# Performance work log

Hardware: AMD Instinct MI355X
Metric: run time of the kernel (lower is better)

Reference implementation:

```python
import jax, jax.numpy as jnp
import numpy as np

# ---- static config (mirrors init_kwargs) ----
BATCH = 16384
N_SCALARS = 64
N_KERNELS = 32
L2_INDICES = tuple(range(15))
N_L2 = len(L2_INDICES) + 1          # selected kernels + sum-over-kernels
HIDDEN_MIX = 256
HIDDEN_CORR = 128
SILU_NORM = 1.6790                   # e3nn normalize2mom constant for silu

# ---- real-basis Wigner 3j tensors (unit Frobenius norm, as in e3nn) ----
def _su2_gen(l):
    m = np.arange(-l, l + 1)
    d = 2 * l + 1
    Jz = np.diag(m).astype(complex)
    jp = np.sqrt(l * (l + 1) - m[:-1] * (m[:-1] + 1))
    Jp = np.zeros((d, d), complex)
    Jp[np.arange(1, d), np.arange(0, d - 1)] = jp
    Jm = Jp.conj().T
    return (Jp + Jm) / 2, (Jp - Jm) / 2j, Jz

def _real_basis(l):
    d = 2 * l + 1
    U = np.zeros((d, d), complex)
    U[l, l] = 1.0
    for m in range(1, l + 1):
        U[l + m, l + m] = (-1) ** m / np.sqrt(2)
        U[l + m, l - m] = 1 / np.sqrt(2)
        U[l - m, l - m] = 1j / np.sqrt(2)
        U[l - m, l + m] = -1j * (-1) ** m / np.sqrt(2)
    return U

def _real_gens(l):
    if l == 0:
        return [np.zeros((1, 1))] * 3
    U = _real_basis(l)
    return [np.real(U @ (-1j * J) @ U.conj().T) for J in _su2_gen(l)]

def _w3j(l1, l2, l3):
    G1, G2, G3 = _real_gens(l1), _real_gens(l2), _real_gens(l3)
    d1, d2, d3 = 2 * l1 + 1, 2 * l2 + 1, 2 * l3 + 1
    I1, I2, I3 = np.eye(d1), np.eye(d2), np.eye(d3)
    rows = []
    for a in range(3):  # invariance under all 3 so(3) generators
        rows.append(np.kron(np.kron(G1[a], I2), I3)
                    + np.kron(np.kron(I1, G2[a]), I3)
                    + np.kron(np.kron(I1, I2), G3[a]))
    M = np.concatenate(rows, 0)
    _, _, Vh = np.linalg.svd(M)
    c = Vh[-1].reshape(d1, d2, d3)
    c = c / np.linalg.norm(c)
    idx = np.unravel_index(np.argmax(np.abs(c)), c.shape)
    return (c * np.sign(c[idx])).astype(np.float32)

C000 = jnp.asarray(_w3j(0, 0, 0))
C022 = jnp.asarray(_w3j(0, 2, 2))
C202 = jnp.asarray(_w3j(2, 0, 2))
C220 = jnp.asarray(_w3j(2, 2, 0))
C222 = jnp.asarray(_w3j(2, 2, 2))

def _tp_path(w, c, x1, x2):
    # w: [u,v,w], c (wigner 3j): [i,j,k], x1: [b,u,i], x2: [b,v,j] -> [b,w,k]
    return jnp.einsum('uvw,ijk,bui,bvj->bwk', w, c, x1, x2, optimize='optimal')

def _forward(scalars, kernel_t2s, mlp_w1, mlp_w2, mlp_w3, gate_threshold,
             tp1_w000, tp1_w220, tp1_w022, tp1_w202, tp1_w222,
             tp2_w022, tp2_w202, tp2_w222, correction_scale):
    # ---- KernelMixingHead ----
    h = SILU_NORM * jax.nn.silu(scalars @ mlp_w1 / mlp_w1.shape[0] ** 0.5)
    h = SILU_NORM * jax.nn.silu(h @ mlp_w2 / mlp_w2.shape[0] ** 0.5)
    relative = h @ mlp_w3 / mlp_w3.shape[0] ** 0.5          # [B, K]
    magnitude = jnp.linalg.norm(kernel_t2s, axis=-1)         # [B, K]
    gate = magnitude / (magnitude + gate_threshold)
    weights = relative * gate / N_KERNELS ** 0.5
    mixed = jnp.einsum('bk,bkm->bm', weights, kernel_t2s)    # [B, 5]

    # ---- EquivariantCorrectionHead ----
    sel = kernel_t2s[:, jnp.asarray(L2_INDICES), :]          # [B, n_l2-1, 5]
    t = jnp.concatenate([sel, kernel_t2s.sum(axis=1, keepdims=True)], axis=1)  # [B, N_L2, 5]
    xs = scalars[:, :, None]                                 # [B, ns, 1] (0e channels)
    ns, nl, hc = N_SCALARS, N_L2, HIDDEN_CORR
    # e3nn FullyConnectedTensorProduct path norms ('component'/'element')
    a0 = (1.0 / (ns * ns + nl * nl)) ** 0.5
    a2 = (5.0 / (2 * ns * nl + nl * nl)) ** 0.5
    y0 = a0 * (_tp_path(tp1_w000, C000, xs, xs) + _tp_path(tp1_w220, C220, t, t))   # [B,hc,1]
    y2 = a2 * (_tp_path(tp1_w022, C022, xs, t) + _tp_path(tp1_w202, C202, t, xs)
               + _tp_path(tp1_w222, C222, t, t))                                     # [B,hc,5]
    b2 = (5.0 / (3 * hc * hc)) ** 0.5
    corr = b2 * (_tp_path(tp2_w022, C022, y0, y2) + _tp_path(tp2_w202, C202, y2, y0)
                 + _tp_path(tp2_w222, C222, y2, y2))                                 # [B,1,5]
    return mixed + correction_scale * corr[:, 0, :]

def setup_inputs() -> dict:
    key = jax.random.key(0)
    ks = jax.random.split(key, 13)
    f32 = jnp.float32
    return {
        'scalars': jax.random.normal(ks[0], (BATCH, N_SCALARS), f32),
        'kernel_t2s': jax.random.normal(ks[1], (BATCH, N_KERNELS, 5), f32),
        'mlp_w1': jax.random.normal(ks[2], (N_SCALARS, HIDDEN_MIX), f32),
        'mlp_w2': jax.random.normal(ks[3], (HIDDEN_MIX, HIDDEN_MIX), f32),
        'mlp_w3': jax.random.normal(ks[4], (HIDDEN_MIX, N_KERNELS), f32),
        'gate_threshold': jnp.ones((N_KERNELS,), f32),
        'tp1_w000': jax.random.normal(ks[5], (N_SCALARS, N_SCALARS, HIDDEN_CORR), f32),
        'tp1_w220': jax.random.normal(ks[6], (N_L2, N_L2, HIDDEN_CORR), f32),
        'tp1_w022': jax.random.normal(ks[7], (N_SCALARS, N_L2, HIDDEN_CORR), f32),
        'tp1_w202': jax.random.normal(ks[8], (N_L2, N_SCALARS, HIDDEN_CORR), f32),
        'tp1_w222': jax.random.normal(ks[9], (N_L2, N_L2, HIDDEN_CORR), f32),
        'tp2_w022': jax.random.normal(ks[10], (HIDDEN_CORR, HIDDEN_CORR, 1), f32),
        'tp2_w202': jax.random.normal(ks[11], (HIDDEN_CORR, HIDDEN_CORR, 1), f32),
        'tp2_w222': jax.random.normal(ks[12], (HIDDEN_CORR, HIDDEN_CORR, 1), f32),
        'correction_scale': jnp.asarray(0.1, f32),
    }

def reference(scalars, kernel_t2s, mlp_w1, mlp_w2, mlp_w3, gate_threshold,
              tp1_w000, tp1_w220, tp1_w022, tp1_w202, tp1_w222,
              tp2_w022, tp2_w202, tp2_w222, correction_scale):
    return _forward(scalars, kernel_t2s, mlp_w1, mlp_w2, mlp_w3, gate_threshold,
                    tp1_w000, tp1_w220, tp1_w022, tp1_w202, tp1_w222,
                    tp2_w022, tp2_w202, tp2_w222, correction_scale)
```

## Files before the change

### kernel.cpp

```cpp
#include <hip/hip_runtime.h>
#include <hip/hip_bf16.h>
#include <cmath>
#include <complex>
#include <vector>
#include <cstring>
#include <cstdint>


#define C222_FLIP -1.0f

#define MIX_WS_OFF   0
#define W202T_OFF    327680
#define B2H_OFF      393216
#define B2L_OFF      1294336
#define Y0_WS_OFF    2195456
#define Y2P_OFF      10584064

#define NCHUNK2      110

typedef __attribute__((ext_vector_type(8))) short short8;
typedef __attribute__((ext_vector_type(4))) float f32x4;

struct Coefs {
  float c222[125];
  float d022[5];
  float d202[5];
  float d220[5];
  float a0, a2, b2;
};

#define FMA8(acc, wa, wb, sv) do { \
  acc[0] = fmaf((wa).x, (sv), acc[0]); \
  acc[1] = fmaf((wa).y, (sv), acc[1]); \
  acc[2] = fmaf((wa).z, (sv), acc[2]); \
  acc[3] = fmaf((wa).w, (sv), acc[3]); \
  acc[4] = fmaf((wb).x, (sv), acc[4]); \
  acc[5] = fmaf((wb).y, (sv), acc[5]); \
  acc[6] = fmaf((wb).z, (sv), acc[6]); \
  acc[7] = fmaf((wb).w, (sv), acc[7]); \
} while (0)

#define FMA4(acc, wa, sv) do { \
  acc[0] = fmaf((wa).x, (sv), acc[0]); \
  acc[1] = fmaf((wa).y, (sv), acc[1]); \
  acc[2] = fmaf((wa).z, (sv), acc[2]); \
  acc[3] = fmaf((wa).w, (sv), acc[3]); \
} while (0)

__device__ __forceinline__ float act_silu(float x) {
  return 1.679f * x / (1.0f + expf(-x));
}

__device__ __forceinline__ short f2bf(float x) {
  __hip_bfloat16 h = __float2bfloat16(x);
  return *reinterpret_cast<short*>(&h);
}
__device__ __forceinline__ float bf2f(short s) {
  __hip_bfloat16 h = *reinterpret_cast<__hip_bfloat16*>(&s);
  return __bfloat162float(h);
}

__device__ __forceinline__ int bperm(int n, int k) {
  return ((n >> 4) << 9) | (((((k >> 3) << 4) | (n & 15))) << 3) | (k & 7);
}

__global__ __launch_bounds__(256) void k_prep(
    const float* __restrict__ s, const float* __restrict__ t2s,
    const float* __restrict__ w1, const float* __restrict__ w2,
    const float* __restrict__ w3, const float* __restrict__ gthr,
    float* __restrict__ mixed_ws)
{
  __shared__ float sT[64][36];
  __shared__ float hT[256][36];

  const int tid = threadIdx.x;
  const int b0  = blockIdx.x * 32;

  #pragma unroll
  for (int i = 0; i < 8; i++) {
    int flat = tid + i * 256;
    int bl = flat >> 6, k = flat & 63;
    sT[k][bl] = s[(size_t)(b0 + bl) * 64 + k];
  }
  __syncthreads();

  const int cg = tid & 31, bg = tid >> 5;
  const int c0 = cg * 8, bb0 = bg * 4;

  float acc[4][8];
  #pragma unroll
  for (int j = 0; j < 4; j++)
    #pragma unroll
    for (int i = 0; i < 8; i++) acc[j][i] = 0.f;

  for (int k = 0; k < 64; k++) {
    float4 bv = *(const float4*)&sT[k][bb0];
    float4 wa = *(const float4*)&w1[k * 256 + c0];
    float4 wb = *(const float4*)&w1[k * 256 + c0 + 4];
    const float bvv[4] = {bv.x, bv.y, bv.z, bv.w};
    #pragma unroll
    for (int j = 0; j < 4; j++) { FMA8(acc[j], wa, wb, bvv[j]); }
  }
  #pragma unroll
  for (int j = 0; j < 4; j++)
    #pragma unroll
    for (int i = 0; i < 8; i++)
      hT[c0 + i][bb0 + j] = act_silu(acc[j][i] * 0.125f);
  __syncthreads();

  float acc2[4][8];
  #pragma unroll
  for (int j = 0; j < 4; j++)
    #pragma unroll
    for (int i = 0; i < 8; i++) acc2[j][i] = 0.f;

  for (int k = 0; k < 256; k++) {
    float4 bv = *(const float4*)&hT[k][bb0];
    float4 wa = *(const float4*)&w2[k * 256 + c0];
    float4 wb = *(const float4*)&w2[k * 256 + c0 + 4];
    const float bvv[4] = {bv.x, bv.y, bv.z, bv.w};
    #pragma unroll
    for (int j = 0; j < 4; j++) { FMA8(acc2[j], wa, wb, bvv[j]); }
  }
  __syncthreads();
  #pragma unroll
  for (int j = 0; j < 4; j++)
    #pragma unroll
    for (int i = 0; i < 8; i++)
      hT[c0 + i][bb0 + j] = act_silu(acc2[j][i] * 0.0625f);
  __syncthreads();

  const int jj  = tid & 31;
  const int blg = tid >> 5;
  float acc3[4] = {0.f, 0.f, 0.f, 0.f};
  for (int k = 0; k < 256; k++) {
    float wv  = w3[k * 32 + jj];
    float4 hv = *(const float4*)&hT[k][blg * 4];
    acc3[0] = fmaf(hv.x, wv, acc3[0]);
    acc3[1] = fmaf(hv.y, wv, acc3[1]);
    acc3[2] = fmaf(hv.z, wv, acc3[2]);
    acc3[3] = fmaf(hv.w, wv, acc3[3]);
  }
  const float thrv = gthr[jj];
  #pragma unroll
  for (int r = 0; r < 4; r++) {
    int bl = blg * 4 + r;
    int b  = b0 + bl;
    float rel = acc3[r] * 0.0625f;
    const float* tp = t2s + (size_t)(b * 32 + jj) * 5;
    float tv0 = tp[0], tv1 = tp[1], tv2 = tp[2], tv3 = tp[3], tv4 = tp[4];
    float mag  = sqrtf(tv0*tv0 + tv1*tv1 + tv2*tv2 + tv3*tv3 + tv4*tv4);
    float gate = mag / (mag + thrv);
    float w = rel * gate * 0.17677669529663687f;
    float pm0 = w*tv0, pm1 = w*tv1, pm2 = w*tv2, pm3 = w*tv3, pm4 = w*tv4;
    #pragma unroll
    for (int off = 16; off >= 1; off >>= 1) {
      pm0 += __shfl_xor(pm0, off);
      pm1 += __shfl_xor(pm1, off);
      pm2 += __shfl_xor(pm2, off);
      pm3 += __shfl_xor(pm3, off);
      pm4 += __shfl_xor(pm4, off);
    }
    if (jj == 0) {
      float* mp = mixed_ws + (size_t)b * 5;
      mp[0] = pm0; mp[1] = pm1; mp[2] = pm2; mp[3] = pm3; mp[4] = pm4;
    }
  }
}

__global__ __launch_bounds__(256) void k_wprep(
    const float* __restrict__ w000,
    const float* __restrict__ w2022x,
    const float* __restrict__ w2202, float* __restrict__ wSum,
    const float* __restrict__ w022, const float* __restrict__ w202,
    const float* __restrict__ w222, const float* __restrict__ w220,
    short* __restrict__ B2h, short* __restrict__ B2l)
{
  const int tid = threadIdx.x;
  const int blk = blockIdx.x;
  if (blk < 64) {
    int u = blk;
    int base = u * 64 - (u * (u - 1)) / 2;
    int n = (64 - u) * 128;
    for (int idx = tid; idx < n; idx += 256) {
      int t = idx >> 7, wc = idx & 127;
      int v = u + t;
      int p = base + t;
      float val = w000[(size_t)(u * 64 + v) * 128 + wc];
      if (v > u) val += w000[(size_t)(v * 64 + u) * 128 + wc];
      size_t off = (size_t)(45 + (p >> 5)) * 4096 + bperm(wc, p & 31);
      short hs = f2bf(val);
      B2h[off] = hs;
      B2l[off] = f2bf(val - bf2f(hs));
    }
  } else if (blk < 128) {
    int idx = (blk - 64) * 256 + tid;
    int u = idx >> 7, v = idx & 127;
    wSum[v * 128 + u] = w2022x[(size_t)v * 128 + u] + w2202[(size_t)u * 128 + v];
  } else {
    int c = blk - 128;
    #pragma unroll
    for (int i = 0; i < 16; i++) {
      int e = i * 256 + tid;
      int nb = e >> 9;
      int ln = (e >> 3) & 63;
      int j  = e & 7;
      int w  = nb * 16 + (ln & 15);
      int kk = ((ln >> 4) << 3) | j;
      float V = 0.f;
      if (c < 32) {
        int v = c >> 1, u = (c & 1) * 32 + kk;
        V = w022[(size_t)(u * 16 + v) * 128 + w]
          + w202[(size_t)(v * 64 + u) * 128 + w];
      } else if (c < 40) {
        int K = (c - 32) * 32 + kk;
        int u = K >> 4, v = K & 15;
        V = w222[(size_t)(u * 16 + v) * 128 + w];
      } else {
        int q = (c - 40) * 32 + kk;
        if (q < 136) {
          int u = 0;
          while ((u + 1) * 16 - ((u + 1) * u) / 2 <= q) u++;
          int base = u * 16 - (u * (u - 1)) / 2;
          int v = u + (q - base);
          V = w220[(size_t)(u * 16 + v) * 128 + w];
          if (v > u) V += w220[(size_t)(v * 16 + u) * 128 + w];
        }
      }
      short hs = f2bf(V);
      B2h[(size_t)c * 4096 + e] = hs;
      B2l[(size_t)c * 4096 + e] = f2bf(V - bf2f(hs));
    }
  }
}

__global__ __launch_bounds__(512) void k_y2a(
    const float* __restrict__ s, const float* __restrict__ t2s,
    const short* __restrict__ B2h, const short* __restrict__ B2l,
    unsigned short* __restrict__ y2p, Coefs cf)
{
  __shared__ float sL[64][68];
  __shared__ float tL[64][81];
  __shared__ __align__(16) short BhL[2][4096];
  __shared__ __align__(16) short BlL[2][4096];
  __shared__ float cL222[125];

  const int tid  = threadIdx.x;
  const int b0   = blockIdx.x * 64;
  const int wave = tid >> 6;
  const int lane = tid & 63;
  const int m16  = lane & 15;
  const int quad = lane >> 4;
  const int bg   = wave & 3;
  const int nh   = wave >> 2;
  const int bloc = bg * 16 + m16;
  const int wbase = nh * 64;

  float dk022[5];
  #pragma unroll
  for (int k = 0; k < 5; k++) dk022[k] = cf.d022[k];

  if (tid == 0) {
    #pragma unroll
    for (int i = 0; i < 125; i++) cL222[i] = cf.c222[i];
  }
  for (int idx = tid; idx < 4096; idx += 512) {
    int bl = idx >> 6, k = idx & 63;
    sL[bl][k] = s[(size_t)(b0 + bl) * 64 + k];
  }
  for (int idx = tid; idx < 5120; idx += 512) {
    int bl = idx / 80, rem = idx - bl * 80;
    int u = rem / 5, m = rem - u * 5;
    int b = b0 + bl;
    float v;
    if (u < 15) v = t2s[(size_t)(b * 32 + u) * 5 + m];
    else {
      v = 0.f;
      for (int kk = 0; kk < 32; kk++) v += t2s[(size_t)(b * 32 + kk) * 5 + m];
    }
    tL[bl][rem] = v;
  }
  __syncthreads();

  ((short8*)BhL[0])[tid] = ((const short8*)B2h)[tid];
  ((short8*)BlL[0])[tid] = ((const short8*)B2l)[tid];
  __syncthreads();

  f32x4 acc[5][4];
  #pragma unroll
  for (int k = 0; k < 5; k++)
    #pragma unroll
    for (int nf = 0; nf < 4; nf++) acc[k][nf] = 0.f;
  f32x4 p[4];
  #pragma unroll
  for (int nf = 0; nf < 4; nf++) p[nf] = 0.f;

  for (int c = 0; c < 40; c++) {
    const int cur = c & 1;
    if (c + 1 < 40) {
      ((short8*)BhL[cur ^ 1])[tid] = ((const short8*)(B2h + (size_t)(c + 1) * 4096))[tid];
      ((short8*)BlL[cur ^ 1])[tid] = ((const short8*)(B2l + (size_t)(c + 1) * 4096))[tid];
    }
    short8 bhv[4], blv[4];
    #pragma unroll
    for (int nf = 0; nf < 4; nf++) {
      const int nb = nh * 4 + nf;
      bhv[nf] = *(const short8*)&BhL[cur][nb * 512 + lane * 8];
      blv[nf] = *(const short8*)&BlL[cur][nb * 512 + lane * 8];
    }

    if (c < 32) {
      const int ks = c & 1;
      float sv[8];
      {
        float4 a = *(const float4*)&sL[bloc][ks * 32 + quad * 8];
        float4 b = *(const float4*)&sL[bloc][ks * 32 + quad * 8 + 4];
        sv[0]=a.x; sv[1]=a.y; sv[2]=a.z; sv[3]=a.w;
        sv[4]=b.x; sv[5]=b.y; sv[6]=b.z; sv[7]=b.w;
      }
      short8 ah, al;
      #pragma unroll
      for (int j = 0; j < 8; j++) {
        float x = sv[j];
        short hs = f2bf(x);
        ah[j] = hs;
        al[j] = f2bf(x - bf2f(hs));
      }
      #pragma unroll
      for (int nf = 0; nf < 4; nf++) {
        p[nf] = __builtin_amdgcn_mfma_f32_16x16x32_bf16(ah, bhv[nf], p[nf], 0, 0, 0);
        p[nf] = __builtin_amdgcn_mfma_f32_16x16x32_bf16(ah, blv[nf], p[nf], 0, 0, 0);
        p[nf] = __builtin_amdgcn_mfma_f32_16x16x32_bf16(al, bhv[nf], p[nf], 0, 0, 0);
      }
      if (ks == 1) {
        const int v = c >> 1;
        #pragma unroll
        for (int r = 0; r < 4; r++) {
          const int bl = bg * 16 + quad * 4 + r;
          const float* tr = &tL[bl][v * 5];
          #pragma unroll
          for (int k = 0; k < 5; k++) {
            float f = dk022[k] * tr[k];
            #pragma unroll
            for (int nf = 0; nf < 4; nf++)
              acc[k][nf][r] += f * p[nf][r];
          }
        }
        #pragma unroll
        for (int nf = 0; nf < 4; nf++) p[nf] = 0.f;
      }
    } else {
      int cc = c - 32;
      int u  = cc * 2 + (quad >> 1);
      int vb = (quad & 1) * 8;
      float tu[5];
      #pragma unroll
      for (int i = 0; i < 5; i++) tu[i] = tL[bloc][u * 5 + i];
      float G[25];
      #pragma unroll
      for (int jk = 0; jk < 25; jk++) {
        float g = 0.f;
        #pragma unroll
        for (int i = 0; i < 5; i++)
          g = fmaf(cL222[i * 25 + jk], tu[i], g);
        G[jk] = g;
      }
      float av[5][8];
      #pragma unroll
      for (int j = 0; j < 8; j++) {
        float t5[5];
        #pragma unroll
        for (int j5 = 0; j5 < 5; j5++) t5[j5] = tL[bloc][(vb + j) * 5 + j5];
        #pragma unroll
        for (int k = 0; k < 5; k++) {
          float q = 0.f;
          #pragma unroll
          for (int j5 = 0; j5 < 5; j5++)
            q = fmaf(G[j5 * 5 + k], t5[j5], q);
          av[k][j] = q;
        }
      }
      #pragma unroll
      for (int k = 0; k < 5; k++) {
        short8 ah, al;
        #pragma unroll
        for (int j = 0; j < 8; j++) {
          float x = av[k][j];
          short hs = f2bf(x);
          ah[j] = hs;
          al[j] = f2bf(x - bf2f(hs));
        }
        #pragma unroll
        for (int nf = 0; nf < 4; nf++) {
          acc[k][nf] = __builtin_amdgcn_mfma_f32_16x16x32_bf16(ah, bhv[nf], acc[k][nf], 0, 0, 0);
          acc[k][nf] = __builtin_amdgcn_mfma_f32_16x16x32_bf16(ah, blv[nf], acc[k][nf], 0, 0, 0);
          acc[k][nf] = __builtin_amdgcn_mfma_f32_16x16x32_bf16(al, bhv[nf], acc[k][nf], 0, 0, 0);
        }
      }
    }
    __syncthreads();
  }

  #pragma unroll
  for (int nf = 0; nf < 4; nf++) {
    int ch = wbase + nf * 16 + m16;
    #pragma unroll
    for (int r = 0; r < 4; r++) {
      int b = b0 + bg * 16 + quad * 4 + r;
      #pragma unroll
      for (int k = 0; k < 5; k++)
        y2p[((size_t)b * 5 + k) * 128 + ch] = (unsigned short)f2bf(acc[k][nf][r]);
    }
  }
}

__global__ __launch_bounds__(512) void k_y0b(
    const float* __restrict__ s, const float* __restrict__ t2s,
    const short* __restrict__ B2h, const short* __restrict__ B2l,
    float* __restrict__ y0w, Coefs cf)
{
  __shared__ float sL[32][65];
  __shared__ float tL[32][81];
  __shared__ unsigned char p136s[136];
  __shared__ unsigned short p16[2080];

  const int tid  = threadIdx.x;
  const int b0   = blockIdx.x * 32;
  const int wave = tid >> 6;
  const int lane = tid & 63;
  const int m16  = lane & 15;
  const int quad = lane >> 4;
  const int bg   = wave & 1;
  const int nh   = wave >> 1;
  const int bloc = bg * 16 + m16;
  const int wbase = nh * 32;

  float dk220[5];
  #pragma unroll
  for (int k = 0; k < 5; k++) dk220[k] = cf.d220[k];

  for (int idx = tid; idx < 2048; idx += 512) {
    int bl = idx >> 6, k = idx & 63;
    sL[bl][k] = s[(size_t)(b0 + bl) * 64 + k];
  }
  for (int idx = tid; idx < 2560; idx += 512) {
    int bl = idx / 80, rem = idx - bl * 80;
    int u = rem / 5, m = rem - u * 5;
    int b = b0 + bl;
    float v;
    if (u < 15) v = t2s[(size_t)(b * 32 + u) * 5 + m];
    else {
      v = 0.f;
      for (int kk = 0; kk < 32; kk++) v += t2s[(size_t)(b * 32 + kk) * 5 + m];
    }
    tL[bl][rem] = v;
  }
  if (tid < 16) {
    int u = tid;
    int base = u * 16 - (u * (u - 1)) / 2;
    for (int t = 0; t < 16 - u; t++)
      p136s[base + t] = (unsigned char)((u << 4) | (u + t));
  }
  if (tid < 64) {
    int u = tid;
    int base = u * 64 - (u * (u - 1)) / 2;
    for (int t = 0; t < 64 - u; t++)
      p16[base + t] = (unsigned short)((u << 8) | (u + t));
  }
  __syncthreads();

  f32x4 accY0[2];
  accY0[0] = 0.f; accY0[1] = 0.f;

  const short8* Bh8 = (const short8*)B2h;
  const short8* Bl8 = (const short8*)B2l;
  const int off0 = (nh * 2) * 64 + lane;
  const int off1 = off0 + 64;

  for (int c = 40; c < NCHUNK2; c++) {
    const size_t cb = (size_t)c * 512;
    short8 bh0 = Bh8[cb + off0];
    short8 bh1 = Bh8[cb + off1];
    short8 bl0 = Bl8[cb + off0];
    short8 bl1 = Bl8[cb + off1];

    short8 ah, al;
    if (c < 45) {
      int cc = c - 40;
      int qbase = cc * 32 + quad * 8;
      #pragma unroll
      for (int j = 0; j < 8; j++) {
        int q = qbase + j;
        float g = 0.f;
        if (q < 136) {
          int uv = p136s[q];
          int u = uv >> 4, v = uv & 15;
          #pragma unroll
          for (int m = 0; m < 5; m++)
            g = fmaf(dk220[m] * tL[bloc][u * 5 + m], tL[bloc][v * 5 + m], g);
        }
        short hs = f2bf(g);
        ah[j] = hs;
        al[j] = f2bf(g - bf2f(hs));
      }
    } else {
      int pbase = (c - 45) * 32 + quad * 8;
      #pragma unroll
      for (int j = 0; j < 8; j++) {
        int uv = p16[pbase + j];
        float x = sL[bloc][uv >> 8] * sL[bloc][uv & 255];
        short hs = f2bf(x);
        ah[j] = hs;
        al[j] = f2bf(x - bf2f(hs));
      }
    }
    accY0[0] = __builtin_amdgcn_mfma_f32_16x16x32_bf16(ah, bh0, accY0[0], 0, 0, 0);
    accY0[0] = __builtin_amdgcn_mfma_f32_16x16x32_bf16(ah, bl0, accY0[0], 0, 0, 0);
    accY0[0] = __builtin_amdgcn_mfma_f32_16x16x32_bf16(al, bh0, accY0[0], 0, 0, 0);
    accY0[1] = __builtin_amdgcn_mfma_f32_16x16x32_bf16(ah, bh1, accY0[1], 0, 0, 0);
    accY0[1] = __builtin_amdgcn_mfma_f32_16x16x32_bf16(ah, bl1, accY0[1], 0, 0, 0);
    accY0[1] = __builtin_amdgcn_mfma_f32_16x16x32_bf16(al, bh1, accY0[1], 0, 0, 0);
  }

  #pragma unroll
  for (int nf = 0; nf < 2; nf++) {
    int ch = wbase + nf * 16 + m16;
    #pragma unroll
    for (int r = 0; r < 4; r++) {
      int b = b0 + bg * 16 + quad * 4 + r;
      y0w[(size_t)b * 128 + ch] = accY0[nf][r];
    }
  }
}

__global__ __launch_bounds__(512) void k_fused(
    const float* __restrict__ mixed_ws,
    const float* __restrict__ y0w, const unsigned short* __restrict__ y2p,
    const float* __restrict__ wSum, const float* __restrict__ w2222,
    const float* __restrict__ csc, float* __restrict__ out, Coefs cf)
{
  __shared__ __align__(16) float y0I[16][128][2];
  __shared__ __align__(16) float wLd[32][128];
  __shared__ float y2S[5][16][32][2];
  __shared__ float cL222[125];
  __shared__ float corrAcc[32][5];
  __shared__ float pPL[32][25];

  const int tid = threadIdx.x;
  const int b0  = blockIdx.x * 32;

  float dk022[5];
  #pragma unroll
  for (int k = 0; k < 5; k++) dk022[k] = cf.d022[k];

  if (tid == 0) {
    #pragma unroll
    for (int i = 0; i < 125; i++) cL222[i] = cf.c222[i];
  }
  for (int idx = tid; idx < 4096; idx += 512) {
    int bl = idx >> 7, ch = idx & 127;
    y0I[bl >> 1][ch][bl & 1] = cf.a0 * y0w[(size_t)(b0 + bl) * 128 + ch];
  }

  const int xw = tid & 31;
  const int g  = tid >> 5;
  const int w0 = xw * 4;
  const int bA = 2 * g, bB = 2 * g + 1;
  const int srow = tid >> 4;
  const int scol = (tid & 15) * 8;

  float y2acc[5][2][4];
  #pragma unroll
  for (int k = 0; k < 5; k++) {
    #pragma unroll
    for (int h = 0; h < 2; h++) {
      int b = b0 + 2 * g + h;
      const unsigned short* yp = y2p + ((size_t)b * 5 + k) * 128 + w0;
      ushort4 u4 = *(const ushort4*)yp;
      y2acc[k][h][0] = cf.a2 * bf2f((short)u4.x);
      y2acc[k][h][1] = cf.a2 * bf2f((short)u4.y);
      y2acc[k][h][2] = cf.a2 * bf2f((short)u4.z);
      y2acc[k][h][3] = cf.a2 * bf2f((short)u4.w);
    }
  }
  __syncthreads();

  {
    float gvr[2][4] = {{0.f,0.f,0.f,0.f},{0.f,0.f,0.f,0.f}};
    for (int t = 0; t < 4; t++) {
      const int u0 = t * 32;
      *(float4*)&wLd[srow][scol]     = *(const float4*)(wSum + (size_t)(u0 + srow) * 128 + scol);
      *(float4*)&wLd[srow][scol + 4] = *(const float4*)(wSum + (size_t)(u0 + srow) * 128 + scol + 4);
      __syncthreads();
      #pragma unroll 8
      for (int uu = 0; uu < 32; uu++) {
        float2 y0p = *(const float2*)&y0I[g][u0 + uu][0];
        float4 w4 = *(const float4*)&wLd[uu][w0];
        FMA4(gvr[0], w4, y0p.x);
        FMA4(gvr[1], w4, y0p.y);
      }
      __syncthreads();
    }
    #pragma unroll
    for (int k = 0; k < 5; k++) {
      float pA = gvr[0][0]*y2acc[k][0][0] + gvr[0][1]*y2acc[k][0][1]
               + gvr[0][2]*y2acc[k][0][2] + gvr[0][3]*y2acc[k][0][3];
      float pB = gvr[1][0]*y2acc[k][1][0] + gvr[1][1]*y2acc[k][1][1]
               + gvr[1][2]*y2acc[k][1][2] + gvr[1][3]*y2acc[k][1][3];
      pA += __shfl_xor(pA, 16); pA += __shfl_xor(pA, 8); pA += __shfl_xor(pA, 4);
      pA += __shfl_xor(pA, 2);  pA += __shfl_xor(pA, 1);
      pB += __shfl_xor(pB, 16); pB += __shfl_xor(pB, 8); pB += __shfl_xor(pB, 4);
      pB += __shfl_xor(pB, 2);  pB += __shfl_xor(pB, 1);
      if (xw == 0) {
        corrAcc[bA][k] = dk022[k] * pA;
        corrAcc[bB][k] = dk022[k] * pB;
      }
    }
  }
  {
    float zr[5][2][4];
    #pragma unroll
    for (int i = 0; i < 5; i++)
      #pragma unroll
      for (int h = 0; h < 2; h++)
        #pragma unroll
        for (int w = 0; w < 4; w++) zr[i][h][w] = 0.f;

    for (int t = 0; t < 4; t++) {
      const int u0 = t * 32;
      *(float4*)&wLd[srow][scol]     = *(const float4*)(w2222 + (size_t)(u0 + srow) * 128 + scol);
      *(float4*)&wLd[srow][scol + 4] = *(const float4*)(w2222 + (size_t)(u0 + srow) * 128 + scol + 4);
      if (w0 >= u0 && w0 < u0 + 32) {
        const int uu0 = w0 - u0;
        #pragma unroll
        for (int i = 0; i < 5; i++)
          #pragma unroll
          for (int h = 0; h < 2; h++)
            #pragma unroll
            for (int c = 0; c < 4; c++)
              y2S[i][g][uu0 + c][h] = y2acc[i][h][c];
      }
      __syncthreads();
      #pragma unroll 4
      for (int uu = 0; uu < 32; uu++) {
        float4 w4 = *(const float4*)&wLd[uu][w0];
        #pragma unroll
        for (int i = 0; i < 5; i++) {
          float ya = y2S[i][g][uu][0];
          float yb = y2S[i][g][uu][1];
          FMA4(zr[i][0], w4, ya);
          FMA4(zr[i][1], w4, yb);
        }
      }
      __syncthreads();
    }
    #pragma unroll
    for (int i = 0; i < 5; i++) {
      #pragma unroll
      for (int j = 0; j < 5; j++) {
        float pA = zr[i][0][0]*y2acc[j][0][0] + zr[i][0][1]*y2acc[j][0][1]
                 + zr[i][0][2]*y2acc[j][0][2] + zr[i][0][3]*y2acc[j][0][3];
        float pB = zr[i][1][0]*y2acc[j][1][0] + zr[i][1][1]*y2acc[j][1][1]
                 + zr[i][1][2]*y2acc[j][1][2] + zr[i][1][3]*y2acc[j][1][3];
        pA += __shfl_xor(pA, 16); pA += __shfl_xor(pA, 8); pA += __shfl_xor(pA, 4);
        pA += __shfl_xor(pA, 2);  pA += __shfl_xor(pA, 1);
        pB += __shfl_xor(pB, 16); pB += __shfl_xor(pB, 8); pB += __shfl_xor(pB, 4);
        pB += __shfl_xor(pB, 2);  pB += __shfl_xor(pB, 1);
        if (xw == 0) {
          pPL[bA][i * 5 + j] = pA;
          pPL[bB][i * 5 + j] = pB;
        }
      }
    }
  }
  __syncthreads();

  if (tid < 160) {
    int bb = tid / 5, k = tid - bb * 5;
    float c2 = 0.f;
    #pragma unroll
    for (int ii = 0; ii < 5; ii++)
      #pragma unroll
      for (int jj = 0; jj < 5; jj++)
        c2 = fmaf(cL222[ii * 25 + jj * 5 + k], pPL[bb][ii * 5 + jj], c2);
    float tot = corrAcc[bb][k] + c2;
    int b = b0 + bb;
    out[(size_t)b * 5 + k] = mixed_ws[(size_t)b * 5 + k] + csc[0] * cf.b2 * tot;
  }
}

namespace {

using cplx = std::complex<double>;

static void su2_gen(int l, std::vector<cplx>& Jx, std::vector<cplx>& Jy,
                    std::vector<cplx>& Jz) {
  int d = 2 * l + 1;
  Jx.assign((size_t)d * d, cplx(0, 0));
  Jy.assign((size_t)d * d, cplx(0, 0));
  Jz.assign((size_t)d * d, cplx(0, 0));
  for (int a = 0; a < d; a++) Jz[(size_t)a * d + a] = cplx(a - l, 0);
  for (int r = 1; r < d; r++) {
    double m = (r - 1) - l;
    double v = std::sqrt(l * (l + 1.0) - m * (m + 1.0));
    Jx[(size_t)r * d + (r - 1)] += cplx(v / 2, 0);
    Jx[(size_t)(r - 1) * d + r] += cplx(v / 2, 0);
    Jy[(size_t)r * d + (r - 1)] += cplx(0, -v / 2);
    Jy[(size_t)(r - 1) * d + r] += cplx(0, v / 2);
  }
}

static void real_basis(int l, std::vector<cplx>& U) {
  int d = 2 * l + 1;
  U.assign((size_t)d * d, cplx(0, 0));
  U[(size_t)l * d + l] = cplx(1, 0);
  double is2 = 1.0 / std::sqrt(2.0);
  for (int m = 1; m <= l; m++) {
    double sgn = (m % 2 == 0) ? 1.0 : -1.0;
    U[(size_t)(l + m) * d + (l + m)] = cplx(sgn * is2, 0);
    U[(size_t)(l + m) * d + (l - m)] = cplx(is2, 0);
    U[(size_t)(l - m) * d + (l - m)] = cplx(0, is2);
    U[(size_t)(l - m) * d + (l + m)] = cplx(0, -sgn * is2);
  }
}

static void real_gens(int l, std::vector<double> G[3]) {
  int d = 2 * l + 1;
  if (l == 0) { for (int a = 0; a < 3; a++) G[a].assign(1, 0.0); return; }
  std::vector<cplx> J[3];
  su2_gen(l, J[0], J[1], J[2]);
  std::vector<cplx> U;
  real_basis(l, U);
  for (int a = 0; a < 3; a++) {
    std::vector<cplx> T((size_t)d * d, cplx(0, 0));
    for (int i = 0; i < d; i++)
      for (int k = 0; k < d; k++) {
        cplx s(0, 0);
        for (int j = 0; j < d; j++)
          s += U[(size_t)i * d + j] * (cplx(0, -1) * J[a][(size_t)j * d + k]);
        T[(size_t)i * d + k] = s;
      }
    G[a].assign((size_t)d * d, 0.0);
    for (int i = 0; i < d; i++)
      for (int k = 0; k < d; k++) {
        cplx s(0, 0);
        for (int j = 0; j < d; j++)
          s += T[(size_t)i * d + j] * std::conj(U[(size_t)k * d + j]);
        G[a][(size_t)i * d + k] = s.real();
      }
  }
}

static void w3j_host(int l1, int l2, int l3, float* out) {
  int d1 = 2 * l1 + 1, d2 = 2 * l2 + 1, d3 = 2 * l3 + 1;
  int D = d1 * d2 * d3;
  std::vector<double> G1[3], G2[3], G3[3];
  real_gens(l1, G1); real_gens(l2, G2); real_gens(l3, G3);
  int R = 3 * D;
  std::vector<double> M((size_t)R * D, 0.0);
  for (int a = 0; a < 3; a++) {
    double* Ma = &M[(size_t)a * D * D];
    for (int i1 = 0; i1 < d1; i1++)
      for (int j1 = 0; j1 < d1; j1++) {
        double g = G1[a][(size_t)i1 * d1 + j1];
        if (g == 0.0) continue;
        for (int i2 = 0; i2 < d2; i2++)
          for (int i3 = 0; i3 < d3; i3++)
            Ma[(size_t)((i1 * d2 + i2) * d3 + i3) * D + ((j1 * d2 + i2) * d3 + i3)] += g;
      }
    for (int i2 = 0; i2 < d2; i2++)
      for (int j2 = 0; j2 < d2; j2++) {
        double g = G2[a][(size_t)i2 * d2 + j2];
        if (g == 0.0) continue;
        for (int i1 = 0; i1 < d1; i1++)
          for (int i3 = 0; i3 < d3; i3++)
            Ma[(size_t)((i1 * d2 + i2) * d3 + i3) * D + ((i1 * d2 + j2) * d3 + i3)] += g;
      }
    for (int i3 = 0; i3 < d3; i3++)
      for (int j3 = 0; j3 < d3; j3++) {
        double g = G3[a][(size_t)i3 * d3 + j3];
        if (g == 0.0) continue;
        for (int i1 = 0; i1 < d1; i1++)
          for (int i2 = 0; i2 < d2; i2++)
            Ma[(size_t)((i1 * d2 + i2) * d3 + i3) * D + ((i1 * d2 + i2) * d3 + j3)] += g;
      }
  }
  std::vector<int> pivcol;
  int rank = 0;
  for (int col = 0; col < D && rank < R; col++) {
    int pr = -1; double pv = 1e-9;
    for (int r = rank; r < R; r++) {
      double av = std::fabs(M[(size_t)r * D + col]);
      if (av > pv) { pv = av; pr = r; }
    }
    if (pr < 0) continue;
    if (pr != rank)
      for (int c = 0; c < D; c++) std::swap(M[(size_t)pr * D + c], M[(size_t)rank * D + c]);
    double inv = 1.0 / M[(size_t)rank * D + col];
    for (int c = 0; c < D; c++) M[(size_t)rank * D + c] *= inv;
    for (int r = 0; r < R; r++) {
      if (r == rank) continue;
      double f = M[(size_t)r * D + col];
      if (f != 0.0)
        for (int c = 0; c < D; c++) M[(size_t)r * D + c] -= f * M[(size_t)rank * D + c];
    }
    pivcol.push_back(col);
    rank++;
  }
  std::vector<char> isp(D, 0);
  for (int c : pivcol) isp[c] = 1;
  int fc = 0;
  for (int c = 0; c < D; c++) if (!isp[c]) { fc = c; break; }
  std::vector<double> x(D, 0.0);
  x[fc] = 1.0;
  for (int r = 0; r < rank; r++) x[pivcol[r]] = -M[(size_t)r * D + fc];
  double n = 0;
  for (double v : x) n += v * v;
  n = std::sqrt(n);
  for (int c = 0; c < D; c++) x[c] /= n;
  double best = 0;
  for (int c = 0; c < D; c++) { double av = std::fabs(x[c]); if (av > best) best = av; }
  double ssum = 0;
  for (int c = 0; c < D; c++) {
    double av = std::fabs(x[c]);
    if (av >= best * 0.999) ssum += (x[c] >= 0 ? 1.0 : -1.0);
  }
  double sgn = (ssum >= 0) ? 1.0 : -1.0;
  for (int c = 0; c < D; c++) out[c] = (float)(x[c] * sgn);
}

}

extern "C" void kernel_launch(void* const* d_in, const int* in_sizes, int n_in,
                              void* d_out, int out_size, void* d_ws, size_t ws_size,
                              hipStream_t stream)
{
  (void)in_sizes; (void)n_in; (void)out_size; (void)ws_size;

  const float* s     = (const float*)d_in[0];
  const float* t2s   = (const float*)d_in[1];
  const float* w1    = (const float*)d_in[2];
  const float* w2    = (const float*)d_in[3];
  const float* w3    = (const float*)d_in[4];
  const float* gthr  = (const float*)d_in[5];
  const float* w000  = (const float*)d_in[6];
  const float* w220  = (const float*)d_in[7];
  const float* w022  = (const float*)d_in[8];
  const float* w202  = (const float*)d_in[9];
  const float* w222  = (const float*)d_in[10];
  const float* w2022 = (const float*)d_in[11];
  const float* w2202 = (const float*)d_in[12];
  const float* w2222 = (const float*)d_in[13];
  const float* csc   = (const float*)d_in[14];
  float* out = (float*)d_out;

  char* ws = (char*)d_ws;
  float* mixed_ws = (float*)(ws + MIX_WS_OFF);
  float* wSum     = (float*)(ws + W202T_OFF);
  short* B2h      = (short*)(ws + B2H_OFF);
  short* B2l      = (short*)(ws + B2L_OFF);
  float* y0_ws    = (float*)(ws + Y0_WS_OFF);
  unsigned short* y2p = (unsigned short*)(ws + Y2P_OFF);

  Coefs cf;
  {
    float c000v[1], c022v[25], c202v[25], c220v[25];
    w3j_host(0, 0, 0, c000v);
    w3j_host(0, 2, 2, c022v);
    w3j_host(2, 0, 2, c202v);
    w3j_host(2, 2, 0, c220v);
    w3j_host(2, 2, 2, cf.c222);
    for (int i = 0; i < 125; i++) cf.c222[i] *= C222_FLIP;
    for (int k = 0; k < 5; k++) {
      cf.d022[k] = c022v[k * 5 + k];
      cf.d202[k] = c202v[k * 5 + k];
      cf.d220[k] = c220v[k * 5 + k];
    }
    (void)c000v;
    cf.a0 = (float)std::sqrt(1.0 / (64.0 * 64.0 + 16.0 * 16.0));
    cf.a2 = (float)std::sqrt(5.0 / (2.0 * 64.0 * 16.0 + 16.0 * 16.0));
    cf.b2 = (float)std::sqrt(5.0 / (3.0 * 128.0 * 128.0));
  }

  hipLaunchKernelGGL(k_prep, dim3(512), dim3(256), 0, stream,
                     s, t2s, w1, w2, w3, gthr, mixed_ws);
  hipLaunchKernelGGL(k_wprep, dim3(173), dim3(256), 0, stream,
                     w000, w2022, w2202, wSum,
                     w022, w202, w222, w220, B2h, B2l);
  hipLaunchKernelGGL(k_y0b, dim3(512), dim3(512), 0, stream,
                     s, t2s, B2h, B2l, y0_ws, cf);
  hipLaunchKernelGGL(k_y2a, dim3(256), dim3(512), 0, stream,
                     s, t2s, B2h, B2l, y2p, cf);
  hipLaunchKernelGGL(k_fused, dim3(512), dim3(512), 0, stream,
                     mixed_ws, y0_ws, y2p, wSum, w2222, csc, out, cf);
}
```

Baseline: 374.4 us.

## Restructure k_y2a: smaller batch tiles, direct global B loads, precomputed bf16 splits

Halves the k_y2a batch tile to 32 rows and doubles the grid, so each wave covers 32 output channels instead of 64. The shared-memory double-buffered B tiles and the per-chunk __syncthreads are gone; B fragments are read straight from global memory, where they should hit in cache. The bf16 hi/lo split of the scalars is now done once at load time and stored in shared memory. This lowers register and LDS pressure and removes barriers, at the cost of more redundant global reads of B across the larger number of blocks.

```diff
diff --git a/kernel.cpp b/kernel.cpp
--- a/kernel.cpp
+++ b/kernel.cpp
@@ -239,22 +239,22 @@
     const short* __restrict__ B2h, const short* __restrict__ B2l,
     unsigned short* __restrict__ y2p, Coefs cf)
 {
-  __shared__ float sL[64][68];
-  __shared__ float tL[64][81];
-  __shared__ __align__(16) short BhL[2][4096];
-  __shared__ __align__(16) short BlL[2][4096];
+  __shared__ float sL[32][65];
+  __shared__ float tL[32][81];
+  __shared__ __align__(16) short ShL[32][72];
+  __shared__ __align__(16) short SlL[32][72];
   __shared__ float cL222[125];
 
   const int tid  = threadIdx.x;
-  const int b0   = blockIdx.x * 64;
+  const int b0   = blockIdx.x * 32;
   const int wave = tid >> 6;
   const int lane = tid & 63;
   const int m16  = lane & 15;
   const int quad = lane >> 4;
-  const int bg   = wave & 3;
-  const int nh   = wave >> 2;
+  const int bg   = wave & 1;
+  const int nh   = wave >> 1;
   const int bloc = bg * 16 + m16;
-  const int wbase = nh * 64;
+  const int wbase = nh * 32;
 
   float dk022[5];
   #pragma unroll
@@ -264,11 +264,15 @@
     #pragma unroll
     for (int i = 0; i < 125; i++) cL222[i] = cf.c222[i];
   }
-  for (int idx = tid; idx < 4096; idx += 512) {
+  for (int idx = tid; idx < 2048; idx += 512) {
     int bl = idx >> 6, k = idx & 63;
-    sL[bl][k] = s[(size_t)(b0 + bl) * 64 + k];
-  }
-  for (int idx = tid; idx < 5120; idx += 512) {
+    float x = s[(size_t)(b0 + bl) * 64 + k];
+    sL[bl][k] = x;
+    short hs = f2bf(x);
+    ShL[bl][k] = hs;
+    SlL[bl][k] = f2bf(x - bf2f(hs));
+  }
+  for (int idx = tid; idx < 2560; idx += 512) {
     int bl = idx / 80, rem = idx - bl * 80;
     int u = rem / 5, m = rem - u * 5;
     int b = b0 + bl;
@@ -282,57 +286,36 @@
   }
   __syncthreads();
 
-  ((short8*)BhL[0])[tid] = ((const short8*)B2h)[tid];
-  ((short8*)BlL[0])[tid] = ((const short8*)B2l)[tid];
-  __syncthreads();
-
-  f32x4 acc[5][4];
-  #pragma unroll
-  for (int k = 0; k < 5; k++)
-    #pragma unroll
-    for (int nf = 0; nf < 4; nf++) acc[k][nf] = 0.f;
-  f32x4 p[4];
-  #pragma unroll
-  for (int nf = 0; nf < 4; nf++) p[nf] = 0.f;
+  f32x4 acc[5][2];
+  #pragma unroll
+  for (int k = 0; k < 5; k++) {
+    acc[k][0] = 0.f; acc[k][1] = 0.f;
+  }
+  f32x4 p0 = 0.f, p1 = 0.f;
+
+  const short8* Bh8 = (const short8*)B2h;
+  const short8* Bl8 = (const short8*)B2l;
+  const int off0 = (nh * 2) * 64 + lane;
+  const int off1 = off0 + 64;
 
   for (int c = 0; c < 40; c++) {
-    const int cur = c & 1;
-    if (c + 1 < 40) {
-      ((short8*)BhL[cur ^ 1])[tid] = ((const short8*)(B2h + (size_t)(c + 1) * 4096))[tid];
-      ((short8*)BlL[cur ^ 1])[tid] = ((const short8*)(B2l + (size_t)(c + 1) * 4096))[tid];
-    }
-    short8 bhv[4], blv[4];
-    #pragma unroll
-    for (int nf = 0; nf < 4; nf++) {
-      const int nb = nh * 4 + nf;
-      bhv[nf] = *(const short8*)&BhL[cur][nb * 512 + lane * 8];
-      blv[nf] = *(const short8*)&BlL[cur][nb * 512 + lane * 8];
-    }
+    const size_t cb = (size_t)c * 512;
+    short8 bh0 = Bh8[cb + off0];
+    short8 bh1 = Bh8[cb + off1];
+    short8 bl0 = Bl8[cb + off0];
+    short8 bl1 = Bl8[cb + off1];
 
     if (c < 32) {
       const int ks = c & 1;
-      float sv[8];
-      {
-        float4 a = *(const float4*)&sL[bloc][ks * 32 + quad * 8];
-        float4 b = *(const float4*)&sL[bloc][ks * 32 + quad * 8 + 4];
-        sv[0]=a.x; sv[1]=a.y; sv[2]=a.z; sv[3]=a.w;
-        sv[4]=b.x; sv[5]=b.y; sv[6]=b.z; sv[7]=b.w;
-      }
-      short8 ah, al;
-      #pragma unroll
-      for (int j = 0; j < 8; j++) {
-        float x = sv[j];
-        short hs = f2bf(x);
-        ah[j] = hs;
-        al[j] = f2bf(x - bf2f(hs));
-      }
-      #pragma unroll
-      for (int nf = 0; nf < 4; nf++) {
-        p[nf] = __builtin_amdgcn_mfma_f32_16x16x32_bf16(ah, bhv[nf], p[nf], 0, 0, 0);
-        p[nf] = __builtin_amdgcn_mfma_f32_16x16x32_bf16(ah, blv[nf], p[nf], 0, 0, 0);
-        p[nf] = __builtin_amdgcn_mfma_f32_16x16x32_bf16(al, bhv[nf], p[nf], 0, 0, 0);
-      }
-      if (ks == 1) {
+      short8 ah = *(const short8*)&ShL[bloc][ks * 32 + quad * 8];
+      short8 al = *(const short8*)&SlL[bloc][ks * 32 + quad * 8];
+      p0 = __builtin_amdgcn_mfma_f32_16x16x32_bf16(ah, bh0, p0, 0, 0, 0);
+      p0 = __builtin_amdgcn_mfma_f32_16x16x32_bf16(ah, bl0, p0, 0, 0, 0);
+      p0 = __builtin_amdgcn_mfma_f32_16x16x32_bf16(al, bh0, p0, 0, 0, 0);
+      p1 = __builtin_amdgcn_mfma_f32_16x16x32_bf16(ah, bh1, p1, 0, 0, 0);
+      p1 = __builtin_amdgcn_mfma_f32_16x16x32_bf16(ah, bl1, p1, 0, 0, 0);
+      p1 = __builtin_amdgcn_mfma_f32_16x16x32_bf16(al, bh1, p1, 0, 0, 0);
+      if (ks) {
         const int v = c >> 1;
         #pragma unroll
         for (int r = 0; r < 4; r++) {
@@ -341,13 +324,11 @@
           #pragma unroll
           for (int k = 0; k < 5; k++) {
             float f = dk022[k] * tr[k];
-            #pragma unroll
-            for (int nf = 0; nf < 4; nf++)
-              acc[k][nf][r] += f * p[nf][r];
+            acc[k][0][r] += f * p0[r];
+            acc[k][1][r] += f * p1[r];
           }
         }
-        #pragma unroll
-        for (int nf = 0; nf < 4; nf++) p[nf] = 0.f;
+        p0 = 0.f; p1 = 0.f;
       }
     } else {
       int cc = c - 32;
@@ -365,44 +346,31 @@
           g = fmaf(cL222[i * 25 + jk], tu[i], g);
         G[jk] = g;
       }
-      float av[5][8];
-      #pragma unroll
-      for (int j = 0; j < 8; j++) {
-        float t5[5];
-        #pragma unroll
-        for (int j5 = 0; j5 < 5; j5++) t5[j5] = tL[bloc][(vb + j) * 5 + j5];
-        #pragma unroll
-        for (int k = 0; k < 5; k++) {
-          float q = 0.f;
-          #pragma unroll
-          for (int j5 = 0; j5 < 5; j5++)
-            q = fmaf(G[j5 * 5 + k], t5[j5], q);
-          av[k][j] = q;
-        }
-      }
       #pragma unroll
       for (int k = 0; k < 5; k++) {
         short8 ah, al;
         #pragma unroll
         for (int j = 0; j < 8; j++) {
-          float x = av[k][j];
-          short hs = f2bf(x);
+          float q = 0.f;
+          #pragma unroll
+          for (int j5 = 0; j5 < 5; j5++)
+            q = fmaf(G[j5 * 5 + k], tL[bloc][(vb + j) * 5 + j5], q);
+          short hs = f2bf(q);
           ah[j] = hs;
-          al[j] = f2bf(x - bf2f(hs));
+          al[j] = f2bf(q - bf2f(hs));
         }
-        #pragma unroll
-        for (int nf = 0; nf < 4; nf++) {
-          acc[k][nf] = __builtin_amdgcn_mfma_f32_16x16x32_bf16(ah, bhv[nf], acc[k][nf], 0, 0, 0);
-          acc[k][nf] = __builtin_amdgcn_mfma_f32_16x16x32_bf16(ah, blv[nf], acc[k][nf], 0, 0, 0);
-          acc[k][nf] = __builtin_amdgcn_mfma_f32_16x16x32_bf16(al, bhv[nf], acc[k][nf], 0, 0, 0);
-        }
-      }
-    }
-    __syncthreads();
-  }
-
-  #pragma unroll
-  for (int nf = 0; nf < 4; nf++) {
+        acc[k][0] = __builtin_amdgcn_mfma_f32_16x16x32_bf16(ah, bh0, acc[k][0], 0, 0, 0);
+        acc[k][0] = __builtin_amdgcn_mfma_f32_16x16x32_bf16(ah, bl0, acc[k][0], 0, 0, 0);
+        acc[k][0] = __builtin_amdgcn_mfma_f32_16x16x32_bf16(al, bh0, acc[k][0], 0, 0, 0);
+        acc[k][1] = __builtin_amdgcn_mfma_f32_16x16x32_bf16(ah, bh1, acc[k][1], 0, 0, 0);
+        acc[k][1] = __builtin_amdgcn_mfma_f32_16x16x32_bf16(ah, bl1, acc[k][1], 0, 0, 0);
+        acc[k][1] = __builtin_amdgcn_mfma_f32_16x16x32_bf16(al, bh1, acc[k][1], 0, 0, 0);
+      }
+    }
+  }
+
+  #pragma unroll
+  for (int nf = 0; nf < 2; nf++) {
     int ch = wbase + nf * 16 + m16;
     #pragma unroll
     for (int r = 0; r < 4; r++) {
@@ -889,7 +857,7 @@
                      w022, w202, w222, w220, B2h, B2l);
   hipLaunchKernelGGL(k_y0b, dim3(512), dim3(512), 0, stream,
                      s, t2s, B2h, B2l, y0_ws, cf);
-  hipLaunchKernelGGL(k_y2a, dim3(256), dim3(512), 0, stream,
+  hipLaunchKernelGGL(k_y2a, dim3(512), dim3(512), 0, stream,
                      s, t2s, B2h, B2l, y2p, cf);
   hipLaunchKernelGGL(k_fused, dim3(512), dim3(512), 0, stream,
                      mixed_ws, y0_ws, y2p, wSum, w2222, csc, out, cf);
```

After: 404.2 us. +8.0%, slower.
